# Kernel tuning notes

Measured on AMD Instinct MI355X. Metric: run time of the kernel, lower is better.

Reference implementation:

```python
import jax, jax.numpy as jnp
import numpy as np

B, T, C, H, W = 1, 7, 128, 64, 64
IC = C // 2
MB = 256  # codebook size (hardcoded in source)


def setup_inputs() -> dict:
    key = jax.random.key(0)
    ks = jax.random.split(key, 15)
    rn = lambda k, s, sc=1.0: sc * jax.random.normal(k, s, dtype=jnp.float32)
    return {
        "x": rn(ks[0], (B, T, C, H, W)),
        "gn_gamma": 1.0 + rn(ks[1], (C,), 0.1),
        "gn_beta": rn(ks[2], (C,), 0.1),
        "g_w": rn(ks[3], (IC, C), 0.05), "g_b": rn(ks[4], (IC,), 0.05),
        "theta_w": rn(ks[5], (IC, C), 0.05), "theta_b": rn(ks[6], (IC,), 0.05),
        "phi_w": rn(ks[7], (IC, C), 0.05), "phi_b": rn(ks[8], (IC,), 0.05),
        "wz_w": rn(ks[9], (C, IC * 7), 0.05), "wz_b": rn(ks[10], (C,), 0.05),
        "wz1_w": rn(ks[11], (C, IC), 0.05), "wz1_b": rn(ks[12], (C,), 0.05),
        "mb": rn(ks[13], (IC, MB)),
        "std": 4.0 * jnp.ones((1,), jnp.float32),
    }


def _groupnorm(v, gamma, beta, groups=32, eps=1e-6):
    # v: (B_, C_, H_, W_)
    b_ = v.shape[0]
    vr = v.reshape(b_, groups, -1)
    mu = vr.mean(axis=-1, keepdims=True)
    var = vr.var(axis=-1, keepdims=True)
    vn = ((vr - mu) * jax.lax.rsqrt(var + eps)).reshape(v.shape)
    return vn * gamma[:, None, None] + beta[:, None, None]


def _conv1x1(v, w, b):
    # v: (B_, Cin, H, W), w: (Cout, Cin)
    return jnp.einsum('bchw,oc->bohw', v, w) + b[:, None, None]


def reference(x, gn_gamma, gn_beta, g_w, g_b, theta_w, theta_b, phi_w, phi_b,
              wz_w, wz_b, wz1_w, wz1_b, mb, std):
    b, t, c, h, w = x.shape
    ic = g_w.shape[0]
    n = h * w

    # distance matrix D[(i,j),(k,l)] = (j-l)^2 + (i-k)^2  (row-major flatten of (i,j))
    yy, xx = jnp.meshgrid(jnp.arange(h), jnp.arange(w), indexing='ij')
    yf = yy.reshape(-1).astype(x.dtype)
    xf = xx.reshape(-1).astype(x.dtype)
    D = (xf[:, None] - xf[None, :]) ** 2 + (yf[:, None] - yf[None, :]) ** 2  # (n, n)
    weight = jnp.exp(-0.5 * D / (std[0] * std[0]))  # (n, n)

    q = x[:, 3]  # (b, c, h, w)
    hn = _groupnorm(x.reshape(b * t, c, h, w), gn_gamma, gn_beta)
    qn = _groupnorm(q, gn_gamma, gn_beta)

    g_x = _conv1x1(hn, g_w, g_b).reshape(b, t, ic, n)
    theta_x = _conv1x1(hn, theta_w, theta_b).reshape(b, t, ic, n)
    phi = _conv1x1(qn, phi_w, phi_b).reshape(b, ic, n).transpose(0, 2, 1)  # (b, n, ic)

    def frame(_, tg):
        theta_t, g_t = tg  # each (b, ic, n)
        f = jnp.einsum('bnc,bcm->bnm', phi, theta_t)        # (b, n, n)
        fdc = jax.nn.softmax(f, axis=-1) * weight            # post-softmax reweight
        y = jnp.einsum('bnm,bcm->bnc', fdc, g_t)            # (b, n, ic)
        return None, y

    _, ys = jax.lax.scan(frame, None,
                         (theta_x.transpose(1, 0, 2, 3), g_x.transpose(1, 0, 2, 3)))
    # ys: (t, b, n, ic) -> (b, t*ic, h, w)
    corr = ys.transpose(1, 0, 3, 2).reshape(b, t * ic, h, w)
    W_y = _conv1x1(corr, wz_w, wz_b)

    # codebook memory attention
    f1 = jnp.einsum('bnc,ck->bnk', phi, mb) * (float(ic) ** -0.5)
    fdc1 = jax.nn.softmax(f1, axis=-1)
    y1 = jnp.einsum('bnk,ck->bnc', fdc1, mb)  # (b, n, ic)
    qloss = jnp.mean(jnp.abs(phi - y1))
    y1 = y1.transpose(0, 2, 1).reshape(b, ic, h, w)
    W_y1 = _conv1x1(y1, wz1_w, wz1_b)

    z = W_y + q + W_y1
    return z, qloss
```

## Files before the change

### kernel.cpp

```cpp
#include <hip/hip_runtime.h>
#include <hip/hip_bf16.h>

#define TT 7
#define CCH 128
#define ICH 64
#define NHW 4096
#define NSPLIT 4
#define MCHUNK (NHW/NSPLIT)

typedef __attribute__((ext_vector_type(8))) short short8;
typedef __attribute__((ext_vector_type(4))) short sshort4;
typedef __attribute__((ext_vector_type(4))) float floatx4;

#define LOG2E 1.44269504f

static __device__ __forceinline__ short f2bf(float f){
  __hip_bfloat16 h = __float2bfloat16(f);
  return *reinterpret_cast<short*>(&h);
}
static __device__ __forceinline__ float bf2f(short s){
  __hip_bfloat16 h = *reinterpret_cast<__hip_bfloat16*>(&s);
  return __bfloat162float(h);
}

__global__ void k_stats(const float* __restrict__ x, float* __restrict__ mu,
                        float* __restrict__ rstd, float* __restrict__ qacc){
  int t = blockIdx.x >> 5, g = blockIdx.x & 31;
  const float* base = x + ((size_t)t*CCH + g*4) * NHW;
  float s = 0.f, s2 = 0.f;
  for (int i = threadIdx.x; i < 4*NHW; i += 256){
    float v = base[i]; s += v; s2 += v*v;
  }
  #pragma unroll
  for (int off = 32; off; off >>= 1){
    s  += __shfl_down(s, off);
    s2 += __shfl_down(s2, off);
  }
  __shared__ float sh[8];
  int w = threadIdx.x >> 6;
  if ((threadIdx.x & 63) == 0){ sh[w] = s; sh[4+w] = s2; }
  __syncthreads();
  if (threadIdx.x == 0){
    float S  = sh[0]+sh[1]+sh[2]+sh[3];
    float S2 = sh[4]+sh[5]+sh[6]+sh[7];
    float m  = S * (1.f/16384.f);
    float var = S2 * (1.f/16384.f) - m*m;
    mu[blockIdx.x]   = m;
    rstd[blockIdx.x] = rsqrtf(var + 1e-6f);
    if (blockIdx.x == 0) qacc[0] = 0.f;
  }
}

__global__ __launch_bounds__(256) void k_cast(const float* __restrict__ x,
                                              __hip_bfloat16* __restrict__ xbf){
  __shared__ short tile[64][136];
  int t = blockIdx.y, n0 = blockIdx.x*64;
  int ln = threadIdx.x & 63, cq = threadIdx.x >> 6;
  #pragma unroll 4
  for (int ci = 0; ci < 32; ++ci){
    int c = cq*32 + ci;
    tile[ln][c] = f2bf(x[((size_t)t*CCH + c)*NHW + n0 + ln]);
  }
  __syncthreads();
  int row = threadIdx.x >> 2, seg = threadIdx.x & 3;
  short* dst = reinterpret_cast<short*>(xbf) + ((size_t)t*NHW + n0 + row)*CCH + seg*32;
  #pragma unroll
  for (int k = 0; k < 4; ++k){
    short8 v;
    #pragma unroll
    for (int j = 0; j < 8; ++j) v[j] = tile[row][seg*32 + k*8 + j];
    *reinterpret_cast<short8*>(dst + k*8) = v;
  }
}

__global__ void k_setup(const float* __restrict__ gw, const float* __restrict__ gb,
                        const float* __restrict__ thw, const float* __restrict__ thb,
                        const float* __restrict__ phw, const float* __restrict__ phb,
                        const float* __restrict__ gamma, const float* __restrict__ beta,
                        const float* __restrict__ mu, const float* __restrict__ rstd,
                        __hip_bfloat16* __restrict__ Wth, float* __restrict__ bth,
                        __hip_bfloat16* __restrict__ Wg,  float* __restrict__ bg,
                        __hip_bfloat16* __restrict__ Wphi, float* __restrict__ bphi,
                        const float* __restrict__ wz, const float* __restrict__ wz1,
                        const float* __restrict__ wz_b, const float* __restrict__ wz1_b,
                        const float* __restrict__ mb,
                        __hip_bfloat16* __restrict__ wzcat, float* __restrict__ biasz,
                        __hip_bfloat16* __restrict__ mbT, __hip_bfloat16* __restrict__ mbbf){
  if (blockIdx.x < 4){
    int idx = blockIdx.x*256 + threadIdx.x;
    if (idx >= 960) return;
    const float *W, *B; __hip_bfloat16 *Wf; float *bfo; int t, o;
    if (idx < 448){ t = idx >> 6; o = idx & 63; W = thw; B = thb; Wf = Wth + ((size_t)t*ICH + o)*CCH; bfo = bth + t*64 + o; }
    else if (idx < 896){ int j = idx - 448; t = j >> 6; o = j & 63; W = gw; B = gb; Wf = Wg + ((size_t)t*ICH + o)*CCH; bfo = bg + t*64 + o; }
    else { t = 3; o = idx - 896; W = phw; B = phb; Wf = Wphi + (size_t)o*CCH; bfo = bphi + o; }
    float bias = B[o];
    for (int c = 0; c < CCH; ++c){
      int g = c >> 2;
      float rs = rstd[t*32+g], m = mu[t*32+g];
      float a = gamma[c]*rs;
      float w = W[o*CCH + c];
      Wf[c] = __float2bfloat16(w * a);
      bias += w * (beta[c] - m*a);
    }
    *bfo = bias;
  } else {
    int idx = (blockIdx.x - 4)*256 + threadIdx.x;
    if (idx < 128*512){
      int o = idx >> 9, k = idx & 511;
      float v = (k < 448) ? wz[o*448 + k] : wz1[o*64 + (k-448)];
      wzcat[idx] = __float2bfloat16(v);
    }
    if (idx < 128) biasz[idx] = wz_b[idx] + wz1_b[idx];
    if (idx < 64*256){
      int c = idx >> 8, j = idx & 255;
      float v = mb[idx];
      mbbf[idx] = __float2bfloat16(v);
      mbT[j*64 + c] = __float2bfloat16(v);
    }
  }
}

__global__ __launch_bounds__(256) void k_conv(const __hip_bfloat16* __restrict__ xbf,
    const __hip_bfloat16* __restrict__ Wth, const float* __restrict__ bth,
    const __hip_bfloat16* __restrict__ Wg,  const float* __restrict__ bg,
    const __hip_bfloat16* __restrict__ Wphi, const float* __restrict__ bphi,
    __hip_bfloat16* __restrict__ thetaT, __hip_bfloat16* __restrict__ g_nat,
    __hip_bfloat16* __restrict__ phi_bf){
  const int t = blockIdx.y, n0 = blockIdx.x*64;
  const int w = threadIdx.x >> 6, lane = threadIdx.x & 63;
  const int l15 = lane & 15, quad = lane >> 4;

  const short* xb = reinterpret_cast<const short*>(xbf) + ((size_t)t*NHW + n0)*CCH;
  short8 B[4][4];
  #pragma unroll
  for (int nt = 0; nt < 4; ++nt)
    #pragma unroll
    for (int kk = 0; kk < 4; ++kk)
      B[nt][kk] = *reinterpret_cast<const short8*>(xb + (size_t)(nt*16 + l15)*CCH + kk*32 + quad*8);

  {
    const short* aw = reinterpret_cast<const short*>(Wth) + ((size_t)t*ICH + w*16 + l15)*CCH + quad*8;
    short8 A[4];
    #pragma unroll
    for (int kk = 0; kk < 4; ++kk) A[kk] = *reinterpret_cast<const short8*>(aw + kk*32);
    float4 bv = *reinterpret_cast<const float4*>(bth + t*64 + w*16 + quad*4);
    #pragma unroll
    for (int nt = 0; nt < 4; ++nt){
      floatx4 acc = (floatx4){0.f,0.f,0.f,0.f};
      #pragma unroll
      for (int kk = 0; kk < 4; ++kk) acc = __builtin_amdgcn_mfma_f32_16x16x32_bf16(A[kk], B[nt][kk], acc, 0, 0, 0);
      sshort4 pk;
      pk[0] = f2bf(acc[0] + bv.x); pk[1] = f2bf(acc[1] + bv.y);
      pk[2] = f2bf(acc[2] + bv.z); pk[3] = f2bf(acc[3] + bv.w);
      short* dst = reinterpret_cast<short*>(thetaT) + ((size_t)t*NHW + n0 + nt*16 + l15)*ICH + w*16 + quad*4;
      *reinterpret_cast<sshort4*>(dst) = pk;
    }
  }
  {
    const short* aw = reinterpret_cast<const short*>(Wg) + ((size_t)t*ICH + w*16 + l15)*CCH + quad*8;
    short8 A[4];
    #pragma unroll
    for (int kk = 0; kk < 4; ++kk) A[kk] = *reinterpret_cast<const short8*>(aw + kk*32);
    float4 bv = *reinterpret_cast<const float4*>(bg + t*64 + w*16 + quad*4);
    #pragma unroll
    for (int nt = 0; nt < 4; ++nt){
      floatx4 acc = (floatx4){0.f,0.f,0.f,0.f};
      #pragma unroll
      for (int kk = 0; kk < 4; ++kk) acc = __builtin_amdgcn_mfma_f32_16x16x32_bf16(A[kk], B[nt][kk], acc, 0, 0, 0);
      short* gb = reinterpret_cast<short*>(g_nat);
      float bvv[4] = {bv.x, bv.y, bv.z, bv.w};
      #pragma unroll
      for (int r = 0; r < 4; ++r)
        gb[((size_t)t*ICH + w*16 + quad*4 + r)*NHW + n0 + nt*16 + l15] = f2bf(acc[r] + bvv[r]);
    }
  }
  if (t == 3){
    const short* aw = reinterpret_cast<const short*>(Wphi) + (size_t)(w*16 + l15)*CCH + quad*8;
    short8 A[4];
    #pragma unroll
    for (int kk = 0; kk < 4; ++kk) A[kk] = *reinterpret_cast<const short8*>(aw + kk*32);
    float4 bv = *reinterpret_cast<const float4*>(bphi + w*16 + quad*4);
    #pragma unroll
    for (int nt = 0; nt < 4; ++nt){
      floatx4 acc = (floatx4){0.f,0.f,0.f,0.f};
      #pragma unroll
      for (int kk = 0; kk < 4; ++kk) acc = __builtin_amdgcn_mfma_f32_16x16x32_bf16(A[kk], B[nt][kk], acc, 0, 0, 0);
      sshort4 pk;
      pk[0] = f2bf(acc[0] + bv.x); pk[1] = f2bf(acc[1] + bv.y);
      pk[2] = f2bf(acc[2] + bv.z); pk[3] = f2bf(acc[3] + bv.w);
      short* dst = reinterpret_cast<short*>(phi_bf) + (size_t)(n0 + nt*16 + l15)*ICH + w*16 + quad*4;
      *reinterpret_cast<sshort4*>(dst) = pk;
    }
  }
}

__global__ __launch_bounds__(256, 4) void k_attn(
    const __hip_bfloat16* __restrict__ phi_bf,
    const __hip_bfloat16* __restrict__ thetaT,
    const __hip_bfloat16* __restrict__ g_nat,
    const float* __restrict__ stdp,
    float* __restrict__ Opart, float* __restrict__ Zpart)
{
  const int t    = blockIdx.z;
  const int sp   = blockIdx.y;
  const int w    = threadIdx.x >> 6;
  const int lane = threadIdx.x & 63;
  const int l15  = lane & 15;
  const int quad = lane >> 4;
  const int n0   = blockIdx.x*64;
  const int yn   = blockIdx.x;

  __shared__ short Plds[2][64][72];
  __shared__ float Zsh[4][64];

  const float sstd = stdp[0];
  const float coef = -0.5f / (sstd*sstd);

  const short* phi_s = reinterpret_cast<const short*>(phi_bf);
  const short* th_s  = reinterpret_cast<const short*>(thetaT) + (size_t)t*NHW*ICH;
  const short* g_s   = reinterpret_cast<const short*>(g_nat)  + (size_t)t*ICH*NHW;

  short8 phB[4][2];
  #pragma unroll
  for (int nt = 0; nt < 4; ++nt){
    const short* pp = phi_s + (size_t)(n0 + nt*16 + l15)*ICH + quad*8;
    phB[nt][0] = *reinterpret_cast<const short8*>(pp);
    phB[nt][1] = *reinterpret_cast<const short8*>(pp + 32);
  }

  float wxv[4][4];
  {
    const int xm = w*16 + quad*4;
    #pragma unroll
    for (int nt = 0; nt < 4; ++nt){
      int xn = nt*16 + l15;
      #pragma unroll
      for (int r = 0; r < 4; ++r){
        int dx = xn - (xm + r);
        wxv[nt][r] = exp2f(coef * LOG2E * (float)(dx*dx));
      }
    }
  }

  const int ci = w >> 1, nj = w & 1;
  floatx4 oacc[2][2];
  #pragma unroll
  for (int a = 0; a < 2; ++a)
    #pragma unroll
    for (int b = 0; b < 2; ++b) oacc[a][b] = (floatx4){0.f,0.f,0.f,0.f};
  float psum[4] = {0.f,0.f,0.f,0.f};

  int m0 = sp*MCHUNK;
  for (int it = 0; it < MCHUNK/64; ++it, m0 += 64){
    const int buf = it & 1;

    short8 gA[2][2];
    #pragma unroll
    for (int ct = 0; ct < 2; ++ct){
      const short* gp = g_s + (size_t)(ci*32 + ct*16 + l15)*NHW + m0 + quad*8;
      gA[ct][0] = *reinterpret_cast<const short8*>(gp);
      gA[ct][1] = *reinterpret_cast<const short8*>(gp + 32);
    }

    const short* tp = th_s + (size_t)(m0 + w*16 + l15)*ICH + quad*8;
    short8 a0 = *reinterpret_cast<const short8*>(tp);
    short8 a1 = *reinterpret_cast<const short8*>(tp + 32);

    floatx4 s[4];
    #pragma unroll
    for (int nt = 0; nt < 4; ++nt){
      floatx4 acc = (floatx4){0.f,0.f,0.f,0.f};
      acc = __builtin_amdgcn_mfma_f32_16x16x32_bf16(a0, phB[nt][0], acc, 0, 0, 0);
      s[nt] = __builtin_amdgcn_mfma_f32_16x16x32_bf16(a1, phB[nt][1], acc, 0, 0, 0);
    }

    const int ym = m0 >> 6;
    const int dy = yn - ym;
    const float wyv = exp2f(coef * LOG2E * (float)(dy*dy));
    #pragma unroll
    for (int nt = 0; nt < 4; ++nt){
      sshort4 pk;
      #pragma unroll
      for (int r = 0; r < 4; ++r){
        float p = exp2f(__builtin_fmaf(s[nt][r], LOG2E, -8.f*LOG2E));
        psum[nt] += p;
        pk[r] = f2bf(p * (wyv * wxv[nt][r]));
      }
      *reinterpret_cast<sshort4*>(&Plds[buf][nt*16 + l15][w*16 + quad*4]) = pk;
    }

    __syncthreads();

    short8 pB[2][2];
    #pragma unroll
    for (int nt2 = 0; nt2 < 2; ++nt2){
      const short* pr = &Plds[buf][nj*32 + nt2*16 + l15][quad*8];
      pB[nt2][0] = *reinterpret_cast<const short8*>(pr);
      pB[nt2][1] = *reinterpret_cast<const short8*>(pr + 32);
    }

    #pragma unroll
    for (int ct = 0; ct < 2; ++ct)
      #pragma unroll
      for (int nt2 = 0; nt2 < 2; ++nt2){
        oacc[ct][nt2] = __builtin_amdgcn_mfma_f32_16x16x32_bf16(gA[ct][0], pB[nt2][0], oacc[ct][nt2], 0, 0, 0);
        oacc[ct][nt2] = __builtin_amdgcn_mfma_f32_16x16x32_bf16(gA[ct][1], pB[nt2][1], oacc[ct][nt2], 0, 0, 0);
      }
  }

  float* Ob = Opart + (size_t)(t*NSPLIT + sp)*ICH*NHW;
  #pragma unroll
  for (int ct = 0; ct < 2; ++ct)
    #pragma unroll
    for (int nt2 = 0; nt2 < 2; ++nt2){
      int c = ci*32 + ct*16 + quad*4;
      int n = n0 + nj*32 + nt2*16 + l15;
      #pragma unroll
      for (int r = 0; r < 4; ++r)
        Ob[(size_t)(c + r)*NHW + n] = oacc[ct][nt2][r];
    }

  #pragma unroll
  for (int nt = 0; nt < 4; ++nt){
    float z = psum[nt];
    z += __shfl_xor(z, 16);
    z += __shfl_xor(z, 32);
    psum[nt] = z;
  }
  if (quad == 0){
    #pragma unroll
    for (int nt = 0; nt < 4; ++nt) Zsh[w][nt*16 + l15] = psum[nt];
  }
  __syncthreads();
  if (threadIdx.x < 64){
    float z = Zsh[0][threadIdx.x] + Zsh[1][threadIdx.x] + Zsh[2][threadIdx.x] + Zsh[3][threadIdx.x];
    Zpart[(size_t)(t*NSPLIT + sp)*NHW + n0 + threadIdx.x] = z;
  }
}

__global__ __launch_bounds__(256) void k_merge(const float* __restrict__ Opart,
    const float* __restrict__ Zpart, __hip_bfloat16* __restrict__ corrT){
  __shared__ short tile[64][72];
  __shared__ float zinv[64];
  const int t = blockIdx.y, n0 = blockIdx.x*64;

  if (threadIdx.x < 64){
    float zs = 0.f;
    #pragma unroll
    for (int s = 0; s < NSPLIT; ++s)
      zs += Zpart[(size_t)(t*NSPLIT + s)*NHW + n0 + threadIdx.x];
    zinv[threadIdx.x] = 1.f / zs;
  }
  __syncthreads();

  const int nq = threadIdx.x & 15, cc = threadIdx.x >> 4;
  #pragma unroll
  for (int cp = 0; cp < 4; ++cp){
    int c = cp*16 + cc;
    float4 acc = {0.f,0.f,0.f,0.f};
    #pragma unroll
    for (int s = 0; s < NSPLIT; ++s){
      float4 v = *reinterpret_cast<const float4*>(
        Opart + ((size_t)(t*NSPLIT + s)*ICH + c)*NHW + n0 + nq*4);
      acc.x += v.x; acc.y += v.y; acc.z += v.z; acc.w += v.w;
    }
    tile[nq*4+0][c] = f2bf(acc.x * zinv[nq*4+0]);
    tile[nq*4+1][c] = f2bf(acc.y * zinv[nq*4+1]);
    tile[nq*4+2][c] = f2bf(acc.z * zinv[nq*4+2]);
    tile[nq*4+3][c] = f2bf(acc.w * zinv[nq*4+3]);
  }
  __syncthreads();

  #pragma unroll
  for (int rep = 0; rep < 2; ++rep){
    int idx = rep*256 + threadIdx.x;
    int n = idx >> 3, seg = idx & 7;
    short8 v = *reinterpret_cast<short8*>(&tile[n][seg*8]);
    *reinterpret_cast<short8*>(reinterpret_cast<short*>(corrT)
        + (size_t)(n0 + n)*512 + t*64 + seg*8) = v;
  }
}

__global__ __launch_bounds__(256) void k_mb(const __hip_bfloat16* __restrict__ phi_bf,
    const __hip_bfloat16* __restrict__ mbT, const __hip_bfloat16* __restrict__ mbbf,
    __hip_bfloat16* __restrict__ corrT, float* __restrict__ qacc){
  const int n0 = blockIdx.x*32;
  const int w = threadIdx.x >> 6, lane = threadIdx.x & 63;
  const int l15 = lane & 15, quad = lane >> 4;

  __shared__ short P[32][264];
  __shared__ float Zsh[4][32];

  const short* phi_s = reinterpret_cast<const short*>(phi_bf);
  const short* mbT_s = reinterpret_cast<const short*>(mbT);
  const short* mb_s  = reinterpret_cast<const short*>(mbbf);

  short8 Bp[2][2];
  #pragma unroll
  for (int nt = 0; nt < 2; ++nt){
    const short* pp = phi_s + (size_t)(n0 + nt*16 + l15)*ICH + quad*8;
    Bp[nt][0] = *reinterpret_cast<const short8*>(pp);
    Bp[nt][1] = *reinterpret_cast<const short8*>(pp + 32);
  }
  float psum[2] = {0.f, 0.f};
  #pragma unroll
  for (int jt = 0; jt < 4; ++jt){
    const short* ap = mbT_s + (size_t)(w*64 + jt*16 + l15)*64 + quad*8;
    short8 A0 = *reinterpret_cast<const short8*>(ap);
    short8 A1 = *reinterpret_cast<const short8*>(ap + 32);
    #pragma unroll
    for (int nt = 0; nt < 2; ++nt){
      floatx4 acc = (floatx4){0.f,0.f,0.f,0.f};
      acc = __builtin_amdgcn_mfma_f32_16x16x32_bf16(A0, Bp[nt][0], acc, 0, 0, 0);
      acc = __builtin_amdgcn_mfma_f32_16x16x32_bf16(A1, Bp[nt][1], acc, 0, 0, 0);
      sshort4 pk;
      #pragma unroll
      for (int r = 0; r < 4; ++r){
        float p = exp2f(acc[r] * (0.125f*LOG2E));
        psum[nt] += p;
        pk[r] = f2bf(p);
      }
      *reinterpret_cast<sshort4*>(&P[nt*16 + l15][w*64 + jt*16 + quad*4]) = pk;
    }
  }
  #pragma unroll
  for (int nt = 0; nt < 2; ++nt){
    float z = psum[nt];
    z += __shfl_xor(z, 16);
    z += __shfl_xor(z, 32);
    if (quad == 0) Zsh[w][nt*16 + l15] = z;
  }
  __syncthreads();

  float ql = 0.f;
  #pragma unroll
  for (int nt = 0; nt < 2; ++nt){
    floatx4 acc = (floatx4){0.f,0.f,0.f,0.f};
    #pragma unroll
    for (int kk = 0; kk < 8; ++kk){
      const short* ap = mb_s + (size_t)(w*16 + l15)*256 + kk*32 + quad*8;
      short8 A = *reinterpret_cast<const short8*>(ap);
      short8 B = *reinterpret_cast<const short8*>(&P[nt*16 + l15][kk*32 + quad*8]);
      acc = __builtin_amdgcn_mfma_f32_16x16x32_bf16(A, B, acc, 0, 0, 0);
    }
    int nn = nt*16 + l15;
    float zt = Zsh[0][nn] + Zsh[1][nn] + Zsh[2][nn] + Zsh[3][nn];
    float rz = 1.f / zt;
    const short* ph = phi_s + (size_t)(n0 + nn)*ICH + w*16 + quad*4;
    sshort4 ph4 = *reinterpret_cast<const sshort4*>(ph);
    sshort4 pk;
    #pragma unroll
    for (int r = 0; r < 4; ++r){
      float y = acc[r] * rz;
      ql += fabsf(bf2f(ph4[r]) - y);
      pk[r] = f2bf(y);
    }
    short* dst = reinterpret_cast<short*>(corrT) + (size_t)(n0 + nn)*512 + 448 + w*16 + quad*4;
    *reinterpret_cast<sshort4*>(dst) = pk;
  }
  #pragma unroll
  for (int off = 32; off; off >>= 1) ql += __shfl_xor(ql, off);
  if (lane == 0) atomicAdd(qacc, ql);
}

__global__ __launch_bounds__(256) void k_z(const __hip_bfloat16* __restrict__ corrT,
    const __hip_bfloat16* __restrict__ wzcat, const float* __restrict__ biasz,
    const float* __restrict__ x, const float* __restrict__ qacc,
    float* __restrict__ out){
  const int n0 = blockIdx.x*16;
  const int w = threadIdx.x >> 6, lane = threadIdx.x & 63;
  const int l15 = lane & 15, quad = lane >> 4;
  const int o0 = blockIdx.y*64 + w*16;

  const short* ct_s = reinterpret_cast<const short*>(corrT) + (size_t)(n0 + l15)*512 + quad*8;
  const short* wz_s = reinterpret_cast<const short*>(wzcat) + (size_t)(o0 + l15)*512 + quad*8;

  floatx4 acc = (floatx4){0.f,0.f,0.f,0.f};
  #pragma unroll
  for (int kk = 0; kk < 16; ++kk){
    short8 A = *reinterpret_cast<const short8*>(wz_s + kk*32);
    short8 B = *reinterpret_cast<const short8*>(ct_s + kk*32);
    acc = __builtin_amdgcn_mfma_f32_16x16x32_bf16(A, B, acc, 0, 0, 0);
  }
  float4 bz = *reinterpret_cast<const float4*>(biasz + o0 + quad*4);
  float bzv[4] = {bz.x, bz.y, bz.z, bz.w};
  #pragma unroll
  for (int r = 0; r < 4; ++r){
    int o = o0 + quad*4 + r;
    int n = n0 + l15;
    float q = x[((size_t)3*CCH + o)*NHW + n];
    out[(size_t)o*NHW + n] = acc[r] + bzv[r] + q;
  }
  if (blockIdx.x == 0 && blockIdx.y == 0 && threadIdx.x == 0)
    out[(size_t)CCH*NHW] = qacc[0] * (1.f/262144.f);
}

extern "C" void kernel_launch(void* const* d_in, const int* in_sizes, int n_in,
                              void* d_out, int out_size, void* d_ws, size_t ws_size,
                              hipStream_t stream){
  const float* x     = (const float*)d_in[0];
  const float* gamma = (const float*)d_in[1];
  const float* beta  = (const float*)d_in[2];
  const float* g_w   = (const float*)d_in[3];
  const float* g_b   = (const float*)d_in[4];
  const float* th_w  = (const float*)d_in[5];
  const float* th_b  = (const float*)d_in[6];
  const float* ph_w  = (const float*)d_in[7];
  const float* ph_b  = (const float*)d_in[8];
  const float* wz_w  = (const float*)d_in[9];
  const float* wz_b  = (const float*)d_in[10];
  const float* wz1_w = (const float*)d_in[11];
  const float* wz1_b = (const float*)d_in[12];
  const float* mb    = (const float*)d_in[13];
  const float* stdp  = (const float*)d_in[14];
  float* out = (float*)d_out;

  char* ws = (char*)d_ws;
  size_t off = 0;
  auto alloc = [&](size_t bytes)->char*{
    char* p = ws + off; off += (bytes + 255) & ~(size_t)255; return p;
  };
  float* mu      = (float*)alloc(224*4);
  float* rstd    = (float*)alloc(224*4);
  float* qacc    = (float*)alloc(4);
  __hip_bfloat16* xbf    = (__hip_bfloat16*)alloc((size_t)TT*NHW*CCH*2);
  __hip_bfloat16* Wth    = (__hip_bfloat16*)alloc((size_t)TT*ICH*CCH*2);
  float* bth             = (float*)alloc(TT*64*4);
  __hip_bfloat16* Wg     = (__hip_bfloat16*)alloc((size_t)TT*ICH*CCH*2);
  float* bg              = (float*)alloc(TT*64*4);
  __hip_bfloat16* Wphi   = (__hip_bfloat16*)alloc((size_t)ICH*CCH*2);
  float* bphi            = (float*)alloc(64*4);
  __hip_bfloat16* wzcat  = (__hip_bfloat16*)alloc((size_t)128*512*2);
  float* biasz           = (float*)alloc(128*4);
  __hip_bfloat16* mbT    = (__hip_bfloat16*)alloc((size_t)256*64*2);
  __hip_bfloat16* mbbf   = (__hip_bfloat16*)alloc((size_t)64*256*2);
  __hip_bfloat16* thetaT = (__hip_bfloat16*)alloc((size_t)TT*NHW*ICH*2);
  __hip_bfloat16* g_nat  = (__hip_bfloat16*)alloc((size_t)TT*NHW*ICH*2);
  __hip_bfloat16* phi_bf = (__hip_bfloat16*)alloc((size_t)NHW*ICH*2);
  __hip_bfloat16* corrT  = (__hip_bfloat16*)alloc((size_t)NHW*512*2);
  float* Opart   = (float*)alloc((size_t)TT*NSPLIT*ICH*NHW*4);
  float* Zpart   = (float*)alloc((size_t)TT*NSPLIT*NHW*4);

  k_stats<<<224, 256, 0, stream>>>(x, mu, rstd, qacc);
  k_cast <<<dim3(64,7), 256, 0, stream>>>(x, xbf);
  k_setup<<<260, 256, 0, stream>>>(g_w, g_b, th_w, th_b, ph_w, ph_b, gamma, beta,
                                   mu, rstd, Wth, bth, Wg, bg, Wphi, bphi,
                                   wz_w, wz1_w, wz_b, wz1_b, mb, wzcat, biasz, mbT, mbbf);
  k_conv <<<dim3(64,7), 256, 0, stream>>>(xbf, Wth, bth, Wg, bg, Wphi, bphi,
                                          thetaT, g_nat, phi_bf);
  k_attn <<<dim3(64,NSPLIT,7), 256, 0, stream>>>(phi_bf, thetaT, g_nat, stdp, Opart, Zpart);
  k_merge<<<dim3(64,7), 256, 0, stream>>>(Opart, Zpart, corrT);
  k_mb   <<<128, 256, 0, stream>>>(phi_bf, mbT, mbbf, corrT, qacc);
  k_z    <<<dim3(256,2), 256, 0, stream>>>(corrT, wzcat, biasz, x, qacc, out);
}
```

Measured before the change: 254.7 us.

## Restructure attention to per-wave key slices and parallelize stats/cast

The attention kernel drops the shared-memory P exchange and barriers. Each wave now keeps its own 16-key slice and a full 64x64 output accumulator, fed by 16x16x16 MFMAs straight from registers, and writes per-wave partials (NSEFF = 8 splits). Group-norm stats are split per channel with atomic accumulation and a memset, and the cast kernel is split across channel halves for more parallelism. The max-subtraction constant in the softmax exponent is removed. This raises register pressure (launch bounds drop to 3) and doubles partial-buffer traffic in the merge, and removing the stabilizing offset risks overflow.

Result: slower. 267.4 us (+5.0%).

```diff
diff --git a/kernel.cpp b/kernel.cpp
--- a/kernel.cpp
+++ b/kernel.cpp
@@ -5,8 +5,9 @@
 #define CCH 128
 #define ICH 64
 #define NHW 4096
-#define NSPLIT 4
+#define NSPLIT 2
 #define MCHUNK (NHW/NSPLIT)
+#define NSEFF (NSPLIT*4)
 
 typedef __attribute__((ext_vector_type(8))) short short8;
 typedef __attribute__((ext_vector_type(4))) short sshort4;
@@ -14,6 +15,17 @@
 
 #define LOG2E 1.44269504f
 
+#if defined(__has_builtin)
+#if __has_builtin(__builtin_amdgcn_mfma_f32_16x16x16bf16_1k)
+#define MFMA16(A,B,C) __builtin_amdgcn_mfma_f32_16x16x16bf16_1k(A,B,C,0,0,0)
+#elif __has_builtin(__builtin_amdgcn_mfma_f32_16x16x16_bf16)
+#define MFMA16(A,B,C) __builtin_amdgcn_mfma_f32_16x16x16_bf16(A,B,C,0,0,0)
+#endif
+#endif
+#ifndef MFMA16
+#define MFMA16(A,B,C) __builtin_amdgcn_mfma_f32_16x16x16bf16_1k(A,B,C,0,0,0)
+#endif
+
 static __device__ __forceinline__ short f2bf(float f){
   __hip_bfloat16 h = __float2bfloat16(f);
   return *reinterpret_cast<short*>(&h);
@@ -23,52 +35,52 @@
   return __bfloat162float(h);
 }
 
-__global__ void k_stats(const float* __restrict__ x, float* __restrict__ mu,
-                        float* __restrict__ rstd, float* __restrict__ qacc){
-  int t = blockIdx.x >> 5, g = blockIdx.x & 31;
-  const float* base = x + ((size_t)t*CCH + g*4) * NHW;
+__global__ __launch_bounds__(256) void k_stats(const float* __restrict__ x,
+                                               float* __restrict__ sacc,
+                                               float* __restrict__ s2acc){
+  int b = blockIdx.x;
+  int t = b >> 7, c = b & 127;
+  const float4* base = reinterpret_cast<const float4*>(x + ((size_t)t*CCH + c)*NHW);
   float s = 0.f, s2 = 0.f;
-  for (int i = threadIdx.x; i < 4*NHW; i += 256){
-    float v = base[i]; s += v; s2 += v*v;
+  #pragma unroll
+  for (int k = 0; k < 4; ++k){
+    float4 v = base[k*256 + threadIdx.x];
+    s  += v.x + v.y + v.z + v.w;
+    s2 += v.x*v.x + v.y*v.y + v.z*v.z + v.w*v.w;
   }
   #pragma unroll
   for (int off = 32; off; off >>= 1){
-    s  += __shfl_down(s, off);
-    s2 += __shfl_down(s2, off);
+    s  += __shfl_xor(s, off);
+    s2 += __shfl_xor(s2, off);
   }
   __shared__ float sh[8];
   int w = threadIdx.x >> 6;
   if ((threadIdx.x & 63) == 0){ sh[w] = s; sh[4+w] = s2; }
   __syncthreads();
   if (threadIdx.x == 0){
-    float S  = sh[0]+sh[1]+sh[2]+sh[3];
-    float S2 = sh[4]+sh[5]+sh[6]+sh[7];
-    float m  = S * (1.f/16384.f);
-    float var = S2 * (1.f/16384.f) - m*m;
-    mu[blockIdx.x]   = m;
-    rstd[blockIdx.x] = rsqrtf(var + 1e-6f);
-    if (blockIdx.x == 0) qacc[0] = 0.f;
+    atomicAdd(&sacc [t*32 + (c>>2)], sh[0]+sh[1]+sh[2]+sh[3]);
+    atomicAdd(&s2acc[t*32 + (c>>2)], sh[4]+sh[5]+sh[6]+sh[7]);
   }
 }
 
 __global__ __launch_bounds__(256) void k_cast(const float* __restrict__ x,
                                               __hip_bfloat16* __restrict__ xbf){
-  __shared__ short tile[64][136];
-  int t = blockIdx.y, n0 = blockIdx.x*64;
+  __shared__ short tile[64][66];
+  int t = blockIdx.y, n0 = blockIdx.x*64, zh = blockIdx.z;
   int ln = threadIdx.x & 63, cq = threadIdx.x >> 6;
   #pragma unroll 4
-  for (int ci = 0; ci < 32; ++ci){
-    int c = cq*32 + ci;
-    tile[ln][c] = f2bf(x[((size_t)t*CCH + c)*NHW + n0 + ln]);
+  for (int ci = 0; ci < 16; ++ci){
+    int cl = cq*16 + ci;
+    tile[ln][cl] = f2bf(x[((size_t)t*CCH + zh*64 + cl)*NHW + n0 + ln]);
   }
   __syncthreads();
   int row = threadIdx.x >> 2, seg = threadIdx.x & 3;
-  short* dst = reinterpret_cast<short*>(xbf) + ((size_t)t*NHW + n0 + row)*CCH + seg*32;
-  #pragma unroll
-  for (int k = 0; k < 4; ++k){
+  short* dst = reinterpret_cast<short*>(xbf) + ((size_t)t*NHW + n0 + row)*CCH + zh*64 + seg*16;
+  #pragma unroll
+  for (int k = 0; k < 2; ++k){
     short8 v;
     #pragma unroll
-    for (int j = 0; j < 8; ++j) v[j] = tile[row][seg*32 + k*8 + j];
+    for (int j = 0; j < 8; ++j) v[j] = tile[row][seg*16 + k*8 + j];
     *reinterpret_cast<short8*>(dst + k*8) = v;
   }
 }
@@ -77,7 +89,7 @@
                         const float* __restrict__ thw, const float* __restrict__ thb,
                         const float* __restrict__ phw, const float* __restrict__ phb,
                         const float* __restrict__ gamma, const float* __restrict__ beta,
-                        const float* __restrict__ mu, const float* __restrict__ rstd,
+                        const float* __restrict__ sacc, const float* __restrict__ s2acc,
                         __hip_bfloat16* __restrict__ Wth, float* __restrict__ bth,
                         __hip_bfloat16* __restrict__ Wg,  float* __restrict__ bg,
                         __hip_bfloat16* __restrict__ Wphi, float* __restrict__ bphi,
@@ -96,7 +108,9 @@
     float bias = B[o];
     for (int c = 0; c < CCH; ++c){
       int g = c >> 2;
-      float rs = rstd[t*32+g], m = mu[t*32+g];
+      float m  = sacc [t*32+g] * (1.f/16384.f);
+      float vr = s2acc[t*32+g] * (1.f/16384.f) - m*m;
+      float rs = rsqrtf(vr + 1e-6f);
       float a = gamma[c]*rs;
       float w = W[o*CCH + c];
       Wf[c] = __float2bfloat16(w * a);
@@ -194,7 +208,7 @@
   }
 }
 
-__global__ __launch_bounds__(256, 4) void k_attn(
+__global__ __launch_bounds__(256, 3) void k_attn(
     const __hip_bfloat16* __restrict__ phi_bf,
     const __hip_bfloat16* __restrict__ thetaT,
     const __hip_bfloat16* __restrict__ g_nat,
@@ -210,11 +224,8 @@
   const int n0   = blockIdx.x*64;
   const int yn   = blockIdx.x;
 
-  __shared__ short Plds[2][64][72];
-  __shared__ float Zsh[4][64];
-
-  const float sstd = stdp[0];
-  const float coef = -0.5f / (sstd*sstd);
+  const float sstd  = stdp[0];
+  const float coefL = -0.5f / (sstd*sstd) * LOG2E;
 
   const short* phi_s = reinterpret_cast<const short*>(phi_bf);
   const short* th_s  = reinterpret_cast<const short*>(thetaT) + (size_t)t*NHW*ICH;
@@ -237,34 +248,34 @@
       #pragma unroll
       for (int r = 0; r < 4; ++r){
         int dx = xn - (xm + r);
-        wxv[nt][r] = exp2f(coef * LOG2E * (float)(dx*dx));
+        wxv[nt][r] = exp2f(coefL * (float)(dx*dx));
       }
     }
   }
 
-  const int ci = w >> 1, nj = w & 1;
-  floatx4 oacc[2][2];
-  #pragma unroll
-  for (int a = 0; a < 2; ++a)
-    #pragma unroll
-    for (int b = 0; b < 2; ++b) oacc[a][b] = (floatx4){0.f,0.f,0.f,0.f};
+  floatx4 oacc[4][4];
+  #pragma unroll
+  for (int a = 0; a < 4; ++a)
+    #pragma unroll
+    for (int b = 0; b < 4; ++b) oacc[a][b] = (floatx4){0.f,0.f,0.f,0.f};
   float psum[4] = {0.f,0.f,0.f,0.f};
 
-  int m0 = sp*MCHUNK;
-  for (int it = 0; it < MCHUNK/64; ++it, m0 += 64){
-    const int buf = it & 1;
-
-    short8 gA[2][2];
-    #pragma unroll
-    for (int ct = 0; ct < 2; ++ct){
-      const short* gp = g_s + (size_t)(ci*32 + ct*16 + l15)*NHW + m0 + quad*8;
-      gA[ct][0] = *reinterpret_cast<const short8*>(gp);
-      gA[ct][1] = *reinterpret_cast<const short8*>(gp + 32);
-    }
-
-    const short* tp = th_s + (size_t)(m0 + w*16 + l15)*ICH + quad*8;
-    short8 a0 = *reinterpret_cast<const short8*>(tp);
-    short8 a1 = *reinterpret_cast<const short8*>(tp + 32);
+  const int mbeg = sp*MCHUNK;
+  const short* thp = th_s + (size_t)(mbeg + w*16 + l15)*ICH + quad*8;
+  const short* gp0 = g_s + (size_t)( 0 + l15)*NHW + mbeg + w*16 + quad*4;
+  const short* gp1 = g_s + (size_t)(16 + l15)*NHW + mbeg + w*16 + quad*4;
+  const short* gp2 = g_s + (size_t)(32 + l15)*NHW + mbeg + w*16 + quad*4;
+  const short* gp3 = g_s + (size_t)(48 + l15)*NHW + mbeg + w*16 + quad*4;
+
+  const int ymb = mbeg >> 6;
+  for (int it = 0; it < MCHUNK/64; ++it){
+    short8 a0 = *reinterpret_cast<const short8*>(thp);
+    short8 a1 = *reinterpret_cast<const short8*>(thp + 32);
+    thp += 64*ICH;
+    sshort4 ga0 = *reinterpret_cast<const sshort4*>(gp0); gp0 += 64;
+    sshort4 ga1 = *reinterpret_cast<const sshort4*>(gp1); gp1 += 64;
+    sshort4 ga2 = *reinterpret_cast<const sshort4*>(gp2); gp2 += 64;
+    sshort4 ga3 = *reinterpret_cast<const sshort4*>(gp3); gp3 += 64;
 
     floatx4 s[4];
     #pragma unroll
@@ -274,52 +285,40 @@
       s[nt] = __builtin_amdgcn_mfma_f32_16x16x32_bf16(a1, phB[nt][1], acc, 0, 0, 0);
     }
 
-    const int ym = m0 >> 6;
-    const int dy = yn - ym;
-    const float wyv = exp2f(coef * LOG2E * (float)(dy*dy));
-    #pragma unroll
-    for (int nt = 0; nt < 4; ++nt){
-      sshort4 pk;
+    const int dy = yn - (ymb + it);
+    const float wyv = exp2f(coefL * (float)(dy*dy));
+    sshort4 pB[4];
+    #pragma unroll
+    for (int nt = 0; nt < 4; ++nt){
       #pragma unroll
       for (int r = 0; r < 4; ++r){
-        float p = exp2f(__builtin_fmaf(s[nt][r], LOG2E, -8.f*LOG2E));
+        float p = exp2f(s[nt][r] * LOG2E);
         psum[nt] += p;
-        pk[r] = f2bf(p * (wyv * wxv[nt][r]));
+        pB[nt][r] = f2bf(p * (wyv * wxv[nt][r]));
       }
-      *reinterpret_cast<sshort4*>(&Plds[buf][nt*16 + l15][w*16 + quad*4]) = pk;
-    }
-
-    __syncthreads();
-
-    short8 pB[2][2];
-    #pragma unroll
-    for (int nt2 = 0; nt2 < 2; ++nt2){
-      const short* pr = &Plds[buf][nj*32 + nt2*16 + l15][quad*8];
-      pB[nt2][0] = *reinterpret_cast<const short8*>(pr);
-      pB[nt2][1] = *reinterpret_cast<const short8*>(pr + 32);
-    }
-
-    #pragma unroll
-    for (int ct = 0; ct < 2; ++ct)
-      #pragma unroll
-      for (int nt2 = 0; nt2 < 2; ++nt2){
-        oacc[ct][nt2] = __builtin_amdgcn_mfma_f32_16x16x32_bf16(gA[ct][0], pB[nt2][0], oacc[ct][nt2], 0, 0, 0);
-        oacc[ct][nt2] = __builtin_amdgcn_mfma_f32_16x16x32_bf16(gA[ct][1], pB[nt2][1], oacc[ct][nt2], 0, 0, 0);
-      }
-  }
-
-  float* Ob = Opart + (size_t)(t*NSPLIT + sp)*ICH*NHW;
-  #pragma unroll
-  for (int ct = 0; ct < 2; ++ct)
-    #pragma unroll
-    for (int nt2 = 0; nt2 < 2; ++nt2){
-      int c = ci*32 + ct*16 + quad*4;
-      int n = n0 + nj*32 + nt2*16 + l15;
+    }
+
+    #pragma unroll
+    for (int nt = 0; nt < 4; ++nt){
+      oacc[0][nt] = MFMA16(ga0, pB[nt], oacc[0][nt]);
+      oacc[1][nt] = MFMA16(ga1, pB[nt], oacc[1][nt]);
+      oacc[2][nt] = MFMA16(ga2, pB[nt], oacc[2][nt]);
+      oacc[3][nt] = MFMA16(ga3, pB[nt], oacc[3][nt]);
+    }
+  }
+
+  const int si = t*NSEFF + sp*4 + w;
+  float* Ob = Opart + (size_t)si*ICH*NHW;
+  #pragma unroll
+  for (int ct = 0; ct < 4; ++ct)
+    #pragma unroll
+    for (int nt = 0; nt < 4; ++nt){
+      int c = ct*16 + quad*4;
+      int n = n0 + nt*16 + l15;
       #pragma unroll
       for (int r = 0; r < 4; ++r)
-        Ob[(size_t)(c + r)*NHW + n] = oacc[ct][nt2][r];
-    }
-
+        Ob[(size_t)(c + r)*NHW + n] = oacc[ct][nt][r];
+    }
   #pragma unroll
   for (int nt = 0; nt < 4; ++nt){
     float z = psum[nt];
@@ -329,12 +328,8 @@
   }
   if (quad == 0){
     #pragma unroll
-    for (int nt = 0; nt < 4; ++nt) Zsh[w][nt*16 + l15] = psum[nt];
-  }
-  __syncthreads();
-  if (threadIdx.x < 64){
-    float z = Zsh[0][threadIdx.x] + Zsh[1][threadIdx.x] + Zsh[2][threadIdx.x] + Zsh[3][threadIdx.x];
-    Zpart[(size_t)(t*NSPLIT + sp)*NHW + n0 + threadIdx.x] = z;
+    for (int nt = 0; nt < 4; ++nt)
+      Zpart[(size_t)si*NHW + n0 + nt*16 + l15] = psum[nt];
   }
 }
 
@@ -347,8 +342,8 @@
   if (threadIdx.x < 64){
     float zs = 0.f;
     #pragma unroll
-    for (int s = 0; s < NSPLIT; ++s)
-      zs += Zpart[(size_t)(t*NSPLIT + s)*NHW + n0 + threadIdx.x];
+    for (int s = 0; s < NSEFF; ++s)
+      zs += Zpart[(size_t)(t*NSEFF + s)*NHW + n0 + threadIdx.x];
     zinv[threadIdx.x] = 1.f / zs;
   }
   __syncthreads();
@@ -359,9 +354,9 @@
     int c = cp*16 + cc;
     float4 acc = {0.f,0.f,0.f,0.f};
     #pragma unroll
-    for (int s = 0; s < NSPLIT; ++s){
+    for (int s = 0; s < NSEFF; ++s){
       float4 v = *reinterpret_cast<const float4*>(
-        Opart + ((size_t)(t*NSPLIT + s)*ICH + c)*NHW + n0 + nq*4);
+        Opart + ((size_t)(t*NSEFF + s)*ICH + c)*NHW + n0 + nq*4);
       acc.x += v.x; acc.y += v.y; acc.z += v.z; acc.w += v.w;
     }
     tile[nq*4+0][c] = f2bf(acc.x * zinv[nq*4+0]);
@@ -520,9 +515,10 @@
   auto alloc = [&](size_t bytes)->char*{
     char* p = ws + off; off += (bytes + 255) & ~(size_t)255; return p;
   };
-  float* mu      = (float*)alloc(224*4);
-  float* rstd    = (float*)alloc(224*4);
-  float* qacc    = (float*)alloc(4);
+  float* zbuf    = (float*)alloc(452*4);
+  float* sacc    = zbuf;
+  float* s2acc   = zbuf + 224;
+  float* qacc    = zbuf + 448;
   __hip_bfloat16* xbf    = (__hip_bfloat16*)alloc((size_t)TT*NHW*CCH*2);
   __hip_bfloat16* Wth    = (__hip_bfloat16*)alloc((size_t)TT*ICH*CCH*2);
   float* bth             = (float*)alloc(TT*64*4);
@@ -538,13 +534,14 @@
   __hip_bfloat16* g_nat  = (__hip_bfloat16*)alloc((size_t)TT*NHW*ICH*2);
   __hip_bfloat16* phi_bf = (__hip_bfloat16*)alloc((size_t)NHW*ICH*2);
   __hip_bfloat16* corrT  = (__hip_bfloat16*)alloc((size_t)NHW*512*2);
-  float* Opart   = (float*)alloc((size_t)TT*NSPLIT*ICH*NHW*4);
-  float* Zpart   = (float*)alloc((size_t)TT*NSPLIT*NHW*4);
-
-  k_stats<<<224, 256, 0, stream>>>(x, mu, rstd, qacc);
-  k_cast <<<dim3(64,7), 256, 0, stream>>>(x, xbf);
+  float* Opart   = (float*)alloc((size_t)TT*NSEFF*ICH*NHW*4);
+  float* Zpart   = (float*)alloc((size_t)TT*NSEFF*NHW*4);
+
+  hipMemsetAsync(zbuf, 0, 452*4, stream);
+  k_stats<<<896, 256, 0, stream>>>(x, sacc, s2acc);
+  k_cast <<<dim3(64,7,2), 256, 0, stream>>>(x, xbf);
   k_setup<<<260, 256, 0, stream>>>(g_w, g_b, th_w, th_b, ph_w, ph_b, gamma, beta,
-                                   mu, rstd, Wth, bth, Wg, bg, Wphi, bphi,
+                                   sacc, s2acc, Wth, bth, Wg, bg, Wphi, bphi,
                                    wz_w, wz1_w, wz_b, wz1_b, mb, wzcat, biasz, mbT, mbbf);
   k_conv <<<dim3(64,7), 256, 0, stream>>>(xbf, Wth, bth, Wg, bg, Wphi, bphi,
                                           thetaT, g_nat, phi_bf);
```

## Fuse groupnorm stats into cast, parallelize setup, fold log2e into theta weights

Applied to the files above, without the earlier changes.

The separate stats and cast kernels become one precast kernel that converts x to bf16 and accumulates per-group sums with atomics, so x is read once instead of twice. The setup kernel now gives each output row a whole wavefront with a shuffle reduction, replacing the serial per-thread loop over channels. LOG2E is folded into the theta weights and bias, which removes the FMA and the fixed -8 offset before exp2 in attention; bf16 packing uses paired conversions and the occupancy hint rises from 4 to 6. Dropping the offset and computing variance from atomic sums could affect numerical range and accuracy, and a memset launch is added.

Result: slower. 378.7 us (+48.7%).

```diff
diff --git a/kernel.cpp b/kernel.cpp
--- a/kernel.cpp
+++ b/kernel.cpp
@@ -23,92 +23,93 @@
   return __bfloat162float(h);
 }
 
-__global__ void k_stats(const float* __restrict__ x, float* __restrict__ mu,
-                        float* __restrict__ rstd, float* __restrict__ qacc){
-  int t = blockIdx.x >> 5, g = blockIdx.x & 31;
-  const float* base = x + ((size_t)t*CCH + g*4) * NHW;
-  float s = 0.f, s2 = 0.f;
-  for (int i = threadIdx.x; i < 4*NHW; i += 256){
-    float v = base[i]; s += v; s2 += v*v;
+__global__ __launch_bounds__(256) void k_precast(const float* __restrict__ x,
+    __hip_bfloat16* __restrict__ xbf, float* __restrict__ sacc, float* __restrict__ s2acc){
+  __shared__ short tile[64][66];
+  int t = blockIdx.y, n0 = blockIdx.x*64, zh = blockIdx.z;
+  int ln = threadIdx.x & 63, w = threadIdx.x >> 6;
+  float sl[4] = {0.f,0.f,0.f,0.f}, s2l[4] = {0.f,0.f,0.f,0.f};
+  #pragma unroll 4
+  for (int ci = 0; ci < 16; ++ci){
+    int cl = w*16 + ci;
+    float v = x[((size_t)t*CCH + zh*64 + cl)*NHW + n0 + ln];
+    tile[ln][cl] = f2bf(v);
+    sl[ci>>2]  += v;
+    s2l[ci>>2] += v*v;
   }
   #pragma unroll
   for (int off = 32; off; off >>= 1){
-    s  += __shfl_down(s, off);
-    s2 += __shfl_down(s2, off);
-  }
-  __shared__ float sh[8];
-  int w = threadIdx.x >> 6;
-  if ((threadIdx.x & 63) == 0){ sh[w] = s; sh[4+w] = s2; }
-  __syncthreads();
-  if (threadIdx.x == 0){
-    float S  = sh[0]+sh[1]+sh[2]+sh[3];
-    float S2 = sh[4]+sh[5]+sh[6]+sh[7];
-    float m  = S * (1.f/16384.f);
-    float var = S2 * (1.f/16384.f) - m*m;
-    mu[blockIdx.x]   = m;
-    rstd[blockIdx.x] = rsqrtf(var + 1e-6f);
-    if (blockIdx.x == 0) qacc[0] = 0.f;
-  }
-}
-
-__global__ __launch_bounds__(256) void k_cast(const float* __restrict__ x,
-                                              __hip_bfloat16* __restrict__ xbf){
-  __shared__ short tile[64][136];
-  int t = blockIdx.y, n0 = blockIdx.x*64;
-  int ln = threadIdx.x & 63, cq = threadIdx.x >> 6;
-  #pragma unroll 4
-  for (int ci = 0; ci < 32; ++ci){
-    int c = cq*32 + ci;
-    tile[ln][c] = f2bf(x[((size_t)t*CCH + c)*NHW + n0 + ln]);
+    #pragma unroll
+    for (int g = 0; g < 4; ++g){
+      sl[g]  += __shfl_xor(sl[g],  off);
+      s2l[g] += __shfl_xor(s2l[g], off);
+    }
+  }
+  if (ln == 0){
+    #pragma unroll
+    for (int g = 0; g < 4; ++g){
+      atomicAdd(&sacc [t*32 + zh*16 + w*4 + g], sl[g]);
+      atomicAdd(&s2acc[t*32 + zh*16 + w*4 + g], s2l[g]);
+    }
   }
   __syncthreads();
   int row = threadIdx.x >> 2, seg = threadIdx.x & 3;
-  short* dst = reinterpret_cast<short*>(xbf) + ((size_t)t*NHW + n0 + row)*CCH + seg*32;
-  #pragma unroll
-  for (int k = 0; k < 4; ++k){
+  short* dst = reinterpret_cast<short*>(xbf) + ((size_t)t*NHW + n0 + row)*CCH + zh*64 + seg*16;
+  #pragma unroll
+  for (int k = 0; k < 2; ++k){
     short8 v;
     #pragma unroll
-    for (int j = 0; j < 8; ++j) v[j] = tile[row][seg*32 + k*8 + j];
+    for (int j = 0; j < 8; ++j) v[j] = tile[row][seg*16 + k*8 + j];
     *reinterpret_cast<short8*>(dst + k*8) = v;
   }
 }
 
-__global__ void k_setup(const float* __restrict__ gw, const float* __restrict__ gb,
-                        const float* __restrict__ thw, const float* __restrict__ thb,
-                        const float* __restrict__ phw, const float* __restrict__ phb,
-                        const float* __restrict__ gamma, const float* __restrict__ beta,
-                        const float* __restrict__ mu, const float* __restrict__ rstd,
-                        __hip_bfloat16* __restrict__ Wth, float* __restrict__ bth,
-                        __hip_bfloat16* __restrict__ Wg,  float* __restrict__ bg,
-                        __hip_bfloat16* __restrict__ Wphi, float* __restrict__ bphi,
-                        const float* __restrict__ wz, const float* __restrict__ wz1,
-                        const float* __restrict__ wz_b, const float* __restrict__ wz1_b,
-                        const float* __restrict__ mb,
-                        __hip_bfloat16* __restrict__ wzcat, float* __restrict__ biasz,
-                        __hip_bfloat16* __restrict__ mbT, __hip_bfloat16* __restrict__ mbbf){
-  if (blockIdx.x < 4){
-    int idx = blockIdx.x*256 + threadIdx.x;
-    if (idx >= 960) return;
+__global__ __launch_bounds__(256) void k_setup(
+    const float* __restrict__ gw, const float* __restrict__ gb,
+    const float* __restrict__ thw, const float* __restrict__ thb,
+    const float* __restrict__ phw, const float* __restrict__ phb,
+    const float* __restrict__ gamma, const float* __restrict__ beta,
+    const float* __restrict__ sacc, const float* __restrict__ s2acc,
+    __hip_bfloat16* __restrict__ Wth, float* __restrict__ bth,
+    __hip_bfloat16* __restrict__ Wg,  float* __restrict__ bg,
+    __hip_bfloat16* __restrict__ Wphi, float* __restrict__ bphi,
+    const float* __restrict__ wz, const float* __restrict__ wz1,
+    const float* __restrict__ wz_b, const float* __restrict__ wz1_b,
+    const float* __restrict__ mb,
+    __hip_bfloat16* __restrict__ wzcat, float* __restrict__ biasz,
+    __hip_bfloat16* __restrict__ mbT, __hip_bfloat16* __restrict__ mbbf){
+  if (blockIdx.x < 240){
+    int w = threadIdx.x >> 6, lane = threadIdx.x & 63;
+    int oidx = blockIdx.x*4 + w;
     const float *W, *B; __hip_bfloat16 *Wf; float *bfo; int t, o;
-    if (idx < 448){ t = idx >> 6; o = idx & 63; W = thw; B = thb; Wf = Wth + ((size_t)t*ICH + o)*CCH; bfo = bth + t*64 + o; }
-    else if (idx < 896){ int j = idx - 448; t = j >> 6; o = j & 63; W = gw; B = gb; Wf = Wg + ((size_t)t*ICH + o)*CCH; bfo = bg + t*64 + o; }
-    else { t = 3; o = idx - 896; W = phw; B = phb; Wf = Wphi + (size_t)o*CCH; bfo = bphi + o; }
-    float bias = B[o];
-    for (int c = 0; c < CCH; ++c){
+    float scale = 1.f;
+    if (oidx < 448){ t = oidx >> 6; o = oidx & 63; W = thw; B = thb; Wf = Wth + ((size_t)t*ICH + o)*CCH; bfo = bth + t*64 + o; scale = LOG2E; }
+    else if (oidx < 896){ int j = oidx - 448; t = j >> 6; o = j & 63; W = gw; B = gb; Wf = Wg + ((size_t)t*ICH + o)*CCH; bfo = bg + t*64 + o; }
+    else { t = 3; o = oidx - 896; W = phw; B = phb; Wf = Wphi + (size_t)o*CCH; bfo = bphi + o; }
+    float bp = 0.f;
+    #pragma unroll
+    for (int h = 0; h < 2; ++h){
+      int c = h*64 + lane;
       int g = c >> 2;
-      float rs = rstd[t*32+g], m = mu[t*32+g];
-      float a = gamma[c]*rs;
-      float w = W[o*CCH + c];
-      Wf[c] = __float2bfloat16(w * a);
-      bias += w * (beta[c] - m*a);
-    }
-    *bfo = bias;
+      float m  = sacc [t*32+g] * (1.f/16384.f);
+      float vr = s2acc[t*32+g] * (1.f/16384.f) - m*m;
+      float rs = rsqrtf(vr + 1e-6f);
+      float a  = gamma[c]*rs;
+      float wv = W[o*CCH + c];
+      Wf[c] = __float2bfloat16(wv * a * scale);
+      bp += wv * (beta[c] - m*a);
+    }
+    #pragma unroll
+    for (int off = 32; off; off >>= 1) bp += __shfl_xor(bp, off);
+    if (lane == 0) *bfo = (bp + B[o]) * scale;
   } else {
-    int idx = (blockIdx.x - 4)*256 + threadIdx.x;
-    if (idx < 128*512){
-      int o = idx >> 9, k = idx & 511;
-      float v = (k < 448) ? wz[o*448 + k] : wz1[o*64 + (k-448)];
-      wzcat[idx] = __float2bfloat16(v);
+    int idx = (blockIdx.x - 240)*256 + threadIdx.x;
+    #pragma unroll
+    for (int k = 0; k < 2; ++k){
+      int i = idx + k*32768;
+      int o = i >> 9, kk = i & 511;
+      float v = (kk < 448) ? wz[o*448 + kk] : wz1[o*64 + (kk-448)];
+      wzcat[i] = __float2bfloat16(v);
     }
     if (idx < 128) biasz[idx] = wz_b[idx] + wz1_b[idx];
     if (idx < 64*256){
@@ -194,7 +195,7 @@
   }
 }
 
-__global__ __launch_bounds__(256, 4) void k_attn(
+__global__ __launch_bounds__(256, 6) void k_attn(
     const __hip_bfloat16* __restrict__ phi_bf,
     const __hip_bfloat16* __restrict__ thetaT,
     const __hip_bfloat16* __restrict__ g_nat,
@@ -213,8 +214,8 @@
   __shared__ short Plds[2][64][72];
   __shared__ float Zsh[4][64];
 
-  const float sstd = stdp[0];
-  const float coef = -0.5f / (sstd*sstd);
+  const float sstd  = stdp[0];
+  const float coefL = -0.5f / (sstd*sstd) * LOG2E;
 
   const short* phi_s = reinterpret_cast<const short*>(phi_bf);
   const short* th_s  = reinterpret_cast<const short*>(thetaT) + (size_t)t*NHW*ICH;
@@ -237,7 +238,7 @@
       #pragma unroll
       for (int r = 0; r < 4; ++r){
         int dx = xn - (xm + r);
-        wxv[nt][r] = exp2f(coef * LOG2E * (float)(dx*dx));
+        wxv[nt][r] = exp2f(coefL * (float)(dx*dx));
       }
     }
   }
@@ -276,17 +277,22 @@
 
     const int ym = m0 >> 6;
     const int dy = yn - ym;
-    const float wyv = exp2f(coef * LOG2E * (float)(dy*dy));
+    const float wyv = exp2f(coefL * (float)(dy*dy));
     #pragma unroll
     for (int nt = 0; nt < 4; ++nt){
-      sshort4 pk;
+      float pw[4];
       #pragma unroll
       for (int r = 0; r < 4; ++r){
-        float p = exp2f(__builtin_fmaf(s[nt][r], LOG2E, -8.f*LOG2E));
+        float p = exp2f(s[nt][r]);
         psum[nt] += p;
-        pk[r] = f2bf(p * (wyv * wxv[nt][r]));
+        pw[r] = p * (wyv * wxv[nt][r]);
       }
-      *reinterpret_cast<sshort4*>(&Plds[buf][nt*16 + l15][w*16 + quad*4]) = pk;
+      __hip_bfloat162 lo = __float22bfloat162_rn(make_float2(pw[0], pw[1]));
+      __hip_bfloat162 hi = __float22bfloat162_rn(make_float2(pw[2], pw[3]));
+      uint2 u;
+      u.x = *reinterpret_cast<unsigned*>(&lo);
+      u.y = *reinterpret_cast<unsigned*>(&hi);
+      *reinterpret_cast<uint2*>(&Plds[buf][nt*16 + l15][w*16 + quad*4]) = u;
     }
 
     __syncthreads();
@@ -520,9 +526,10 @@
   auto alloc = [&](size_t bytes)->char*{
     char* p = ws + off; off += (bytes + 255) & ~(size_t)255; return p;
   };
-  float* mu      = (float*)alloc(224*4);
-  float* rstd    = (float*)alloc(224*4);
-  float* qacc    = (float*)alloc(4);
+  float* zbuf    = (float*)alloc(452*4);
+  float* sacc    = zbuf;
+  float* s2acc   = zbuf + 224;
+  float* qacc    = zbuf + 448;
   __hip_bfloat16* xbf    = (__hip_bfloat16*)alloc((size_t)TT*NHW*CCH*2);
   __hip_bfloat16* Wth    = (__hip_bfloat16*)alloc((size_t)TT*ICH*CCH*2);
   float* bth             = (float*)alloc(TT*64*4);
@@ -541,15 +548,15 @@
   float* Opart   = (float*)alloc((size_t)TT*NSPLIT*ICH*NHW*4);
   float* Zpart   = (float*)alloc((size_t)TT*NSPLIT*NHW*4);
 
-  k_stats<<<224, 256, 0, stream>>>(x, mu, rstd, qacc);
-  k_cast <<<dim3(64,7), 256, 0, stream>>>(x, xbf);
-  k_setup<<<260, 256, 0, stream>>>(g_w, g_b, th_w, th_b, ph_w, ph_b, gamma, beta,
-                                   mu, rstd, Wth, bth, Wg, bg, Wphi, bphi,
+  hipMemsetAsync(zbuf, 0, 452*4, stream);
+  k_precast<<<dim3(64,7,2), 256, 0, stream>>>(x, xbf, sacc, s2acc);
+  k_setup<<<368, 256, 0, stream>>>(g_w, g_b, th_w, th_b, ph_w, ph_b, gamma, beta,
+                                   sacc, s2acc, Wth, bth, Wg, bg, Wphi, bphi,
                                    wz_w, wz1_w, wz_b, wz1_b, mb, wzcat, biasz, mbT, mbbf);
-  k_conv <<<dim3(64,7), 256, 0, stream>>>(xbf, Wth, bth, Wg, bg, Wphi, bphi,
-                                          thetaT, g_nat, phi_bf);
-  k_attn <<<dim3(64,NSPLIT,7), 256, 0, stream>>>(phi_bf, thetaT, g_nat, stdp, Opart, Zpart);
+  k_conv<<<dim3(64,7), 256, 0, stream>>>(xbf, Wth, bth, Wg, bg, Wphi, bphi,
+                                         thetaT, g_nat, phi_bf);
+  k_attn<<<dim3(64,NSPLIT,7), 256, 0, stream>>>(phi_bf, thetaT, g_nat, stdp, Opart, Zpart);
   k_merge<<<dim3(64,7), 256, 0, stream>>>(Opart, Zpart, corrT);
-  k_mb   <<<128, 256, 0, stream>>>(phi_bf, mbT, mbbf, corrT, qacc);
-  k_z    <<<dim3(256,2), 256, 0, stream>>>(corrT, wzcat, biasz, x, qacc, out);
-}
+  k_mb  <<<128, 256, 0, stream>>>(phi_bf, mbT, mbbf, corrT, qacc);
+  k_z   <<<dim3(256,2), 256, 0, stream>>>(corrT, wzcat, biasz, x, qacc, out);
+}
```
